# Kernel tuning notes

Hardware: AMD Instinct MI355X
Metric: run time of the kernel (lower is better)

The kernel has to match this reference:

```python
import jax, jax.numpy as jnp
import numpy as np

N_NODES = 100000
N_EDGES = 1600000
IN_F = 128
HID_F = 128
OUT_F = 128
HEAD_HID = 128
HEAD_OUT = 64


def setup_inputs() -> dict:
    key = jax.random.key(0)
    ks = jax.random.split(key, 16)
    glorot = lambda k, i, o: jax.random.normal(k, (i, o), jnp.float32) * (2.0 / (i + o)) ** 0.5
    return {
        "x": jax.random.normal(ks[0], (N_NODES, IN_F), jnp.float32),
        "src": jax.random.randint(ks[1], (N_EDGES,), 0, N_NODES),
        "dst": jax.random.randint(ks[2], (N_EDGES,), 0, N_NODES),
        "eps1": jnp.zeros((), jnp.float32),
        "eps2": jnp.zeros((), jnp.float32),
        # mlp_fun1: in_feats -> hid -> hid
        "w11": glorot(ks[3], IN_F, HID_F), "b11": jnp.zeros((HID_F,), jnp.float32),
        "w12": glorot(ks[4], HID_F, HID_F), "b12": jnp.zeros((HID_F,), jnp.float32),
        # mlp_fun2: hid -> hid -> out_feats
        "w21": glorot(ks[5], HID_F, HID_F), "b21": jnp.zeros((HID_F,), jnp.float32),
        "w22": glorot(ks[6], HID_F, OUT_F), "b22": jnp.zeros((OUT_F,), jnp.float32),
        # head mlp: out_feats -> hidden_dim -> output_dim (sigmoid)
        "wm1": glorot(ks[7], OUT_F, HEAD_HID), "bm1": jnp.zeros((HEAD_HID,), jnp.float32),
        "wm2": glorot(ks[8], HEAD_HID, HEAD_OUT), "bm2": jnp.zeros((HEAD_OUT,), jnp.float32),
    }


def _mlp2(h, w1, b1, w2, b2):
    # 2-layer MLP: Linear -> ReLU -> Linear
    return jax.nn.relu(h @ w1 + b1) @ w2 + b2


def _gin_conv(x, src, dst, eps, w1, b1, w2, b2):
    # sum-aggregate over incoming edges, then MLP update (DGL GINConv, learn_eps)
    agg = jax.ops.segment_sum(x[src], dst, num_segments=x.shape[0])  # [N, d]
    return _mlp2((1.0 + eps) * x + agg, w1, b1, w2, b2)


def reference(x, src, dst, eps1, eps2, w11, b11, w12, b12,
              w21, b21, w22, b22, wm1, bm1, wm2, bm2):
    # dropout is identity in eval mode
    h = jax.nn.relu(_gin_conv(x, src, dst, eps1, w11, b11, w12, b12))
    h = jax.nn.relu(_gin_conv(h, src, dst, eps2, w21, b21, w22, b22))
    # head MLP producing per-node probabilities (consumed by log-prob loss)
    return jax.nn.sigmoid(_mlp2(h, wm1, bm1, wm2, bm2))  # [N, output_dim]
```

## Files before the change

kernel.cpp:

```cpp
#include <hip/hip_runtime.h>

static constexpr int NN = 100000;
static constexpr int NE = 1600000;
static constexpr int NBUK = (NN + 255) / 256;
static constexpr int SC_BLOCKS = 400;
static constexpr int SC_CH = NE / SC_BLOCKS;

typedef float     f32x4  __attribute__((ext_vector_type(4)));
typedef _Float16  f16x8  __attribute__((ext_vector_type(8)));

static constexpr float LO_SCALE  = 16384.0f;
static constexpr float LO_USCALE = 1.0f / 16384.0f;

__device__ __forceinline__ unsigned pkh(float x, float y){
  unsigned short a = __builtin_bit_cast(unsigned short, (_Float16)x);
  unsigned short b = __builtin_bit_cast(unsigned short, (_Float16)y);
  return (unsigned)a | ((unsigned)b << 16);
}
__device__ __forceinline__ float2 uph(unsigned u){
  _Float16 a = __builtin_bit_cast(_Float16, (unsigned short)(u & 0xffffu));
  _Float16 b = __builtin_bit_cast(_Float16, (unsigned short)(u >> 16));
  return make_float2((float)a, (float)b);
}

__global__ void k_pack(const float* __restrict__ w11, const float* __restrict__ w12,
                       const float* __restrict__ w21, const float* __restrict__ w22,
                       const float* __restrict__ wm1, const float* __restrict__ wm2,
                       unsigned short* __restrict__ p11, unsigned short* __restrict__ p12,
                       unsigned short* __restrict__ p21, unsigned short* __restrict__ p22,
                       unsigned short* __restrict__ pm1, unsigned short* __restrict__ pm2){
  int b = blockIdx.x, lane = threadIdx.x;
  const float* W; unsigned short* P; int NCT, f;
  if (b < 160){
    int m = b >> 5; f = b & 31; NCT = 8;
    W = (m==0)?w11:(m==1)?w12:(m==2)?w21:(m==3)?w22:wm1;
    P = (m==0)?p11:(m==1)?p12:(m==2)?p21:(m==3)?p22:pm1;
  } else { f = b - 160; NCT = 4; W = wm2; P = pm2; }
  int NC = NCT * 16;
  int kt = f / NCT, ct = f % NCT;
  int hidx = ct >> 2, ct4 = ct & 3;
  int k0 = kt*32 + ((lane>>4)*8), col = ct*16 + (lane&15);
  unsigned short* dh = P + (hidx<<14) + ((kt*4+ct4)<<10) + (lane<<3);
  unsigned short* dl = dh + 512;
  #pragma unroll
  for (int j=0;j<8;j++){
    float v = W[(size_t)(k0+j)*NC + col];
    _Float16 h = (_Float16)v;
    _Float16 l = (_Float16)((v - (float)h) * LO_SCALE);
    dh[j] = __builtin_bit_cast(unsigned short, h);
    dl[j] = __builtin_bit_cast(unsigned short, l);
  }
}

__global__ void k_cvt(const float* __restrict__ x, unsigned* __restrict__ xh, int n4){
  int i = blockIdx.x*256 + threadIdx.x;
  if (i < n4){
    float4 v = reinterpret_cast<const float4*>(x)[i];
    uint2 o; o.x = pkh(v.x, v.y); o.y = pkh(v.z, v.w);
    reinterpret_cast<uint2*>(xh)[i] = o;
  }
}

__global__ __launch_bounds__(256) void k_hist(const int* __restrict__ dst, int* __restrict__ bhist){
  __shared__ int h[NBUK];
  int blk = blockIdx.x, t = threadIdx.x;
  for (int i=t;i<NBUK;i+=256) h[i]=0;
  __syncthreads();
  int e0 = blk*SC_CH;
  for (int e=e0+t; e<e0+SC_CH; e+=256) atomicAdd(&h[((unsigned)dst[e])>>8], 1);
  __syncthreads();
  for (int i=t;i<NBUK;i+=256){ int c=h[i]; if (c) atomicAdd(&bhist[i], c); }
}

__global__ void k_boff2(const int* __restrict__ bhist, int* __restrict__ boff){
  __shared__ int s[512];
  int t = threadIdx.x;
  int v = (t < NBUK) ? bhist[t] : 0;
  s[t] = v; __syncthreads();
  for (int off=1; off<512; off<<=1){
    int u = 0; if (t>=off) u = s[t-off];
    __syncthreads(); s[t] += u; __syncthreads();
  }
  if (t < NBUK) boff[t] = s[t] - v;
}

__global__ __launch_bounds__(256) void k_scatter1(const int* __restrict__ src,
                                                  const int* __restrict__ dst,
                                                  const int* __restrict__ boff,
                                                  int* __restrict__ gbcur,
                                                  uint2* __restrict__ tmp){
  __shared__ int hc[NBUK];
  __shared__ int hb[NBUK];
  int blk = blockIdx.x, t = threadIdx.x;
  int e0 = blk * SC_CH, e1 = e0 + SC_CH;
  for (int i=t;i<NBUK;i+=256) hc[i]=0;
  __syncthreads();
  for (int e=e0+t; e<e1; e+=256) atomicAdd(&hc[((unsigned)dst[e])>>8], 1);
  __syncthreads();
  for (int i=t;i<NBUK;i+=256){ int c = hc[i]; hb[i] = c ? atomicAdd(&gbcur[i], c) : 0; }
  __syncthreads();
  for (int i=t;i<NBUK;i+=256) hc[i]=0;
  __syncthreads();
  for (int e=e0+t; e<e1; e+=256){
    int d = dst[e]; int b = ((unsigned)d)>>8;
    int pos = atomicAdd(&hc[b], 1);
    tmp[(size_t)boff[b] + hb[b] + pos] = make_uint2((unsigned)src[e], (unsigned)d);
  }
}

__global__ __launch_bounds__(256) void k_fill2(const uint2* __restrict__ tmp,
                                               const int* __restrict__ boff,
                                               const int* __restrict__ bhist,
                                               int* __restrict__ eidx,
                                               int* __restrict__ rs, int* __restrict__ deg, int N){
  __shared__ int lh[256];
  __shared__ int ls[256];
  __shared__ int lc[256];
  int b = blockIdx.x, t = threadIdx.x;
  int base = boff[b], cnt = bhist[b];
  int nb0 = b*256;
  lh[t] = 0; lc[t] = 0;
  __syncthreads();
  for (int i=t; i<cnt; i+=256) atomicAdd(&lh[(int)tmp[(size_t)base+i].y - nb0], 1);
  __syncthreads();
  int v = lh[t];
  ls[t] = v; __syncthreads();
  for (int off=1; off<256; off<<=1){
    int u = 0; if (t>=off) u = ls[t-off];
    __syncthreads(); ls[t] += u; __syncthreads();
  }
  int node = nb0 + t;
  if (node < N){ deg[node] = v; rs[node] = base + ls[t] - v; }
  __syncthreads();
  for (int i=t; i<cnt; i+=256){
    uint2 e = tmp[(size_t)base+i];
    int local = (int)e.y - nb0;
    int pos = atomicAdd(&lc[local], 1);
    eidx[base + ls[local] - lh[local] + pos] = (int)e.x;
  }
}

__global__ __launch_bounds__(256) void k_agg(const unsigned* __restrict__ inp,
                                             unsigned* __restrict__ out,
                                             const float* __restrict__ epsp,
                                             const int* __restrict__ rs, const int* __restrict__ deg,
                                             const int* __restrict__ eidx, int N){
  int gw = (blockIdx.x*256 + threadIdx.x) >> 6;
  int lane = threadIdx.x & 63;
  if (gw >= N) return;
  float sc = 1.0f + *epsp;
  float2 v = uph(inp[(size_t)gw*64 + lane]);
  float a0 = sc * v.x, a1 = sc * v.y;
  int beg = rs[gw], d = deg[gw];
  int i = 0;
  for (; i+8 <= d; i += 8){
    unsigned u[8];
    #pragma unroll
    for (int j=0;j<8;j++) u[j] = inp[(size_t)eidx[beg+i+j]*64 + lane];
    #pragma unroll
    for (int j=0;j<8;j++){ float2 f = uph(u[j]); a0 += f.x; a1 += f.y; }
  }
  for (; i < d; ++i){
    float2 u = uph(inp[(size_t)eidx[beg+i]*64 + lane]);
    a0 += u.x; a1 += u.y;
  }
  out[(size_t)gw*64 + lane] = pkh(a0, a1);
}

static constexpr int HSTR = 136;
static constexpr int WSLICE = 32*HSTR;

__device__ __forceinline__ void load_a_glob2(const _Float16* __restrict__ t, int rbase,
                                             int lane, int N, f16x8 a[2][4]){
  #pragma unroll
  for (int ms=0; ms<2; ++ms){
    int row = rbase + ms*16 + (lane & 15); if (row >= N) row = N - 1;
    const _Float16* ap = t + (size_t)row*128 + ((lane>>4)*8);
    #pragma unroll
    for (int kt=0;kt<4;kt++) a[ms][kt] = *reinterpret_cast<const f16x8*>(ap + kt*32);
  }
}
__device__ __forceinline__ void load_a_lds2(const _Float16* slice, int lane, f16x8 a[2][4]){
  int ko = (lane>>4)*8;
  #pragma unroll
  for (int ms=0; ms<2; ++ms){
    const _Float16* rp = slice + (ms*16 + (lane&15))*HSTR + ko;
    #pragma unroll
    for (int kt=0;kt<4;kt++) a[ms][kt] = *reinterpret_cast<const f16x8*>(rp + kt*32);
  }
}

__device__ __forceinline__ void half_relu(const f16x8 a[2][4],
                                          const unsigned short* __restrict__ w,
                                          const float* __restrict__ bias,
                                          _Float16* slice, int lane, int hidx){
  const unsigned short* wb = w + (hidx<<14);
  int r0 = (lane>>4)*4, col0 = lane & 15;
  #pragma unroll
  for (int ct4=0; ct4<4; ++ct4){
    f32x4 c0={0.f,0.f,0.f,0.f}, c1={0.f,0.f,0.f,0.f};
    f32x4 d0={0.f,0.f,0.f,0.f}, d1={0.f,0.f,0.f,0.f};
    #pragma unroll
    for (int kt=0; kt<4; ++kt){
      const f16x8 bh = *reinterpret_cast<const f16x8*>(wb + ((kt*4+ct4)<<10) + (lane<<3));
      const f16x8 bl = *reinterpret_cast<const f16x8*>(wb + ((kt*4+ct4)<<10) + 512 + (lane<<3));
      c0 = __builtin_amdgcn_mfma_f32_16x16x32_f16(a[0][kt], bh, c0, 0,0,0);
      c1 = __builtin_amdgcn_mfma_f32_16x16x32_f16(a[1][kt], bh, c1, 0,0,0);
      d0 = __builtin_amdgcn_mfma_f32_16x16x32_f16(a[0][kt], bl, d0, 0,0,0);
      d1 = __builtin_amdgcn_mfma_f32_16x16x32_f16(a[1][kt], bl, d1, 0,0,0);
    }
    float bv = bias[hidx*64 + ct4*16 + col0];
    int cb = hidx*64 + ct4*16 + col0;
    #pragma unroll
    for (int r=0;r<4;r++){
      float v0 = fmaxf(c0[r] + d0[r]*LO_USCALE + bv, 0.f);
      float v1 = fmaxf(c1[r] + d1[r]*LO_USCALE + bv, 0.f);
      slice[(r0+r)*HSTR + cb]      = (_Float16)v0;
      slice[(16+r0+r)*HSTR + cb]   = (_Float16)v1;
    }
  }
}

__device__ __forceinline__ void head_sig(const f16x8 a[2][4],
                                         const unsigned short* __restrict__ w,
                                         const float* __restrict__ bias,
                                         float* fs, int lane){
  int r0 = (lane>>4)*4, col0 = lane & 15;
  #pragma unroll
  for (int ct4=0; ct4<4; ++ct4){
    f32x4 c0={0.f,0.f,0.f,0.f}, c1={0.f,0.f,0.f,0.f};
    f32x4 d0={0.f,0.f,0.f,0.f}, d1={0.f,0.f,0.f,0.f};
    #pragma unroll
    for (int kt=0; kt<4; ++kt){
      const f16x8 bh = *reinterpret_cast<const f16x8*>(w + ((kt*4+ct4)<<10) + (lane<<3));
      const f16x8 bl = *reinterpret_cast<const f16x8*>(w + ((kt*4+ct4)<<10) + 512 + (lane<<3));
      c0 = __builtin_amdgcn_mfma_f32_16x16x32_f16(a[0][kt], bh, c0, 0,0,0);
      c1 = __builtin_amdgcn_mfma_f32_16x16x32_f16(a[1][kt], bh, c1, 0,0,0);
      d0 = __builtin_amdgcn_mfma_f32_16x16x32_f16(a[0][kt], bl, d0, 0,0,0);
      d1 = __builtin_amdgcn_mfma_f32_16x16x32_f16(a[1][kt], bl, d1, 0,0,0);
    }
    float bv = bias[ct4*16 + col0];
    int cb = ct4*16 + col0;
    #pragma unroll
    for (int r=0;r<4;r++){
      float z0 = c0[r] + d0[r]*LO_USCALE + bv;
      float z1 = c1[r] + d1[r]*LO_USCALE + bv;
      fs[(r0+r)*68 + cb]    = 1.0f / (1.0f + __expf(-z0));
      fs[(16+r0+r)*68 + cb] = 1.0f / (1.0f + __expf(-z1));
    }
  }
}

__global__ __launch_bounds__(256) void k_mlp1(const _Float16* __restrict__ t,
    const unsigned short* __restrict__ w1, const float* __restrict__ b1,
    const unsigned short* __restrict__ w2, const float* __restrict__ b2,
    unsigned* __restrict__ h, int N){
  __shared__ _Float16 lds[4*WSLICE];
  int tid = threadIdx.x, lane = tid & 63, wv = tid >> 6;
  _Float16* slice = lds + wv*WSLICE;
  int rbase = blockIdx.x*128 + wv*32;
  f16x8 a[2][4];
  load_a_glob2(t, rbase, lane, N, a);
  half_relu(a, w1, b1, slice, lane, 0);
  half_relu(a, w1, b1, slice, lane, 1);
  load_a_lds2(slice, lane, a);
  half_relu(a, w2, b2, slice, lane, 0);
  half_relu(a, w2, b2, slice, lane, 1);
  for (int i=lane; i < 32*32; i += 64){
    int r = i >> 5, c = i & 31;
    if (rbase + r < N)
      reinterpret_cast<uint2*>(h)[(size_t)(rbase + r)*32 + c] =
        *reinterpret_cast<const uint2*>(slice + r*HSTR + c*4);
  }
}

__global__ __launch_bounds__(256) void k_mlp2_head(const _Float16* __restrict__ t,
    const unsigned short* __restrict__ w1, const float* __restrict__ b1,
    const unsigned short* __restrict__ w2, const float* __restrict__ b2,
    const unsigned short* __restrict__ w3, const float* __restrict__ b3,
    const unsigned short* __restrict__ w4, const float* __restrict__ b4,
    float* __restrict__ out, int N){
  __shared__ _Float16 lds[4*WSLICE];
  int tid = threadIdx.x, lane = tid & 63, wv = tid >> 6;
  _Float16* slice = lds + wv*WSLICE;
  int rbase = blockIdx.x*128 + wv*32;
  f16x8 a[2][4];
  load_a_glob2(t, rbase, lane, N, a);
  half_relu(a, w1, b1, slice, lane, 0);
  half_relu(a, w1, b1, slice, lane, 1);
  load_a_lds2(slice, lane, a);
  half_relu(a, w2, b2, slice, lane, 0);
  half_relu(a, w2, b2, slice, lane, 1);
  load_a_lds2(slice, lane, a);
  half_relu(a, w3, b3, slice, lane, 0);
  half_relu(a, w3, b3, slice, lane, 1);
  load_a_lds2(slice, lane, a);
  float* fs = reinterpret_cast<float*>(slice);
  head_sig(a, w4, b4, fs, lane);
  for (int i=lane; i < 32*16; i += 64){
    int r = i >> 4, c = i & 15;
    if (rbase + r < N)
      reinterpret_cast<float4*>(out)[(size_t)(rbase + r)*16 + c] =
        *reinterpret_cast<const float4*>(fs + r*68 + c*4);
  }
}

extern "C" void kernel_launch(void* const* d_in, const int* in_sizes, int n_in,
                              void* d_out, int out_size, void* d_ws, size_t ws_size,
                              hipStream_t stream) {
  const float* x   = (const float*)d_in[0];
  const int*   src = (const int*)  d_in[1];
  const int*   dst = (const int*)  d_in[2];
  const float* eps1= (const float*)d_in[3];
  const float* eps2= (const float*)d_in[4];
  const float* w11 = (const float*)d_in[5];  const float* b11 = (const float*)d_in[6];
  const float* w12 = (const float*)d_in[7];  const float* b12 = (const float*)d_in[8];
  const float* w21 = (const float*)d_in[9];  const float* b21 = (const float*)d_in[10];
  const float* w22 = (const float*)d_in[11]; const float* b22 = (const float*)d_in[12];
  const float* wm1 = (const float*)d_in[13]; const float* bm1 = (const float*)d_in[14];
  const float* wm2 = (const float*)d_in[15]; const float* bm2 = (const float*)d_in[16];

  char* ws = (char*)d_ws;
  size_t off = 0;
  auto alloc = [&](size_t bytes) -> void* {
    void* p = ws + off;
    off = (off + bytes + 255) & ~(size_t)255;
    return p;
  };
  unsigned* xh  = (unsigned*)alloc((size_t)NN*64*4);
  unsigned* B0  = (unsigned*)alloc((size_t)NN*64*4);
  unsigned* h1h = (unsigned*)alloc((size_t)NN*64*4);
  uint2* tmp = (uint2*)alloc((size_t)NE*8);
  int* eidx = (int*)alloc((size_t)NE*4);
  int* deg  = (int*)alloc((size_t)NN*4);
  int* rs   = (int*)alloc((size_t)NN*4);
  int* bhist= (int*)alloc((size_t)NBUK*4);
  int* boff = (int*)alloc((size_t)NBUK*4);
  int* gbcur= (int*)alloc((size_t)NBUK*4);
  unsigned short* p11 = (unsigned short*)alloc(128*128*2*2);
  unsigned short* p12 = (unsigned short*)alloc(128*128*2*2);
  unsigned short* p21 = (unsigned short*)alloc(128*128*2*2);
  unsigned short* p22 = (unsigned short*)alloc(128*128*2*2);
  unsigned short* pm1 = (unsigned short*)alloc(128*128*2*2);
  unsigned short* pm2 = (unsigned short*)alloc(128*64*2*2);
  if (off > ws_size) return;

  hipMemsetAsync(bhist, 0, (size_t)NBUK*4, stream);
  hipMemsetAsync(gbcur, 0, (size_t)NBUK*4, stream);

  k_pack<<<176, 64, 0, stream>>>(w11,w12,w21,w22,wm1,wm2, p11,p12,p21,p22,pm1,pm2);
  k_cvt<<<(NN*32 + 255)/256, 256, 0, stream>>>(x, xh, NN*32);
  k_hist<<<SC_BLOCKS, 256, 0, stream>>>(dst, bhist);
  k_boff2<<<1, 512, 0, stream>>>(bhist, boff);
  k_scatter1<<<SC_BLOCKS, 256, 0, stream>>>(src, dst, boff, gbcur, tmp);
  k_fill2<<<NBUK, 256, 0, stream>>>(tmp, boff, bhist, eidx, rs, deg, NN);

  int mgrid = (NN + 127) / 128;
  k_agg<<<(NN+3)/4, 256, 0, stream>>>(xh, B0, eps1, rs, deg, eidx, NN);
  k_mlp1<<<mgrid, 256, 0, stream>>>((const _Float16*)B0, p11, b11, p12, b12, h1h, NN);
  k_agg<<<(NN+3)/4, 256, 0, stream>>>(h1h, B0, eps2, rs, deg, eidx, NN);
  k_mlp2_head<<<mgrid, 256, 0, stream>>>((const _Float16*)B0, p21, b21, p22, b22,
                                         pm1, bm1, pm2, bm2, (float*)d_out, NN);
}
```

Before: 301.2 us.

## Fuse neighbor aggregation into MLP kernels and pack scatter entries to 32 bits

Each wave now gathers and sums neighbor rows for its 32 nodes directly into its LDS slice, then runs the MLP on that slice. This removes the separate aggregation kernels and the fp16 intermediate buffer round trip through global memory. The scatter temp array also packs src<<8 with the low 8 bits of dst into one 32-bit word, halving that traffic. The trade-off is fewer waves doing the latency-bound gather: one wave per 32 nodes instead of one per node, serialized over m, which may expose memory latency.

```diff
diff --git a/kernel.cpp b/kernel.cpp
--- a/kernel.cpp
+++ b/kernel.cpp
@@ -88,7 +88,7 @@
                                                   const int* __restrict__ dst,
                                                   const int* __restrict__ boff,
                                                   int* __restrict__ gbcur,
-                                                  uint2* __restrict__ tmp){
+                                                  unsigned* __restrict__ tmp){
   __shared__ int hc[NBUK];
   __shared__ int hb[NBUK];
   int blk = blockIdx.x, t = threadIdx.x;
@@ -102,13 +102,13 @@
   for (int i=t;i<NBUK;i+=256) hc[i]=0;
   __syncthreads();
   for (int e=e0+t; e<e1; e+=256){
-    int d = dst[e]; int b = ((unsigned)d)>>8;
+    unsigned d = (unsigned)dst[e]; unsigned b = d>>8;
     int pos = atomicAdd(&hc[b], 1);
-    tmp[(size_t)boff[b] + hb[b] + pos] = make_uint2((unsigned)src[e], (unsigned)d);
-  }
-}
-
-__global__ __launch_bounds__(256) void k_fill2(const uint2* __restrict__ tmp,
+    tmp[(size_t)boff[b] + hb[b] + pos] = ((unsigned)src[e] << 8) | (d & 255u);
+  }
+}
+
+__global__ __launch_bounds__(256) void k_fill2(const unsigned* __restrict__ tmp,
                                                const int* __restrict__ boff,
                                                const int* __restrict__ bhist,
                                                int* __restrict__ eidx,
@@ -118,10 +118,9 @@
   __shared__ int lc[256];
   int b = blockIdx.x, t = threadIdx.x;
   int base = boff[b], cnt = bhist[b];
-  int nb0 = b*256;
   lh[t] = 0; lc[t] = 0;
   __syncthreads();
-  for (int i=t; i<cnt; i+=256) atomicAdd(&lh[(int)tmp[(size_t)base+i].y - nb0], 1);
+  for (int i=t; i<cnt; i+=256) atomicAdd(&lh[tmp[(size_t)base+i] & 255u], 1);
   __syncthreads();
   int v = lh[t];
   ls[t] = v; __syncthreads();
@@ -129,29 +128,25 @@
     int u = 0; if (t>=off) u = ls[t-off];
     __syncthreads(); ls[t] += u; __syncthreads();
   }
-  int node = nb0 + t;
+  int node = b*256 + t;
   if (node < N){ deg[node] = v; rs[node] = base + ls[t] - v; }
   __syncthreads();
   for (int i=t; i<cnt; i+=256){
-    uint2 e = tmp[(size_t)base+i];
-    int local = (int)e.y - nb0;
+    unsigned e = tmp[(size_t)base+i];
+    int local = e & 255u;
     int pos = atomicAdd(&lc[local], 1);
-    eidx[base + ls[local] - lh[local] + pos] = (int)e.x;
-  }
-}
-
-__global__ __launch_bounds__(256) void k_agg(const unsigned* __restrict__ inp,
-                                             unsigned* __restrict__ out,
-                                             const float* __restrict__ epsp,
-                                             const int* __restrict__ rs, const int* __restrict__ deg,
-                                             const int* __restrict__ eidx, int N){
-  int gw = (blockIdx.x*256 + threadIdx.x) >> 6;
-  int lane = threadIdx.x & 63;
-  if (gw >= N) return;
-  float sc = 1.0f + *epsp;
-  float2 v = uph(inp[(size_t)gw*64 + lane]);
+    eidx[base + ls[local] - lh[local] + pos] = (int)(e >> 8);
+  }
+}
+
+static constexpr int HSTR = 136;
+static constexpr int WSLICE = 32*HSTR;
+
+__device__ __forceinline__ float2 gather_row(const unsigned* __restrict__ inp, float sc,
+                                             int beg, int d, const int* __restrict__ eidx,
+                                             int node, int lane){
+  float2 v = uph(inp[(size_t)node*64 + lane]);
   float a0 = sc * v.x, a1 = sc * v.y;
-  int beg = rs[gw], d = deg[gw];
   int i = 0;
   for (; i+8 <= d; i += 8){
     unsigned u[8];
@@ -164,22 +159,24 @@
     float2 u = uph(inp[(size_t)eidx[beg+i]*64 + lane]);
     a0 += u.x; a1 += u.y;
   }
-  out[(size_t)gw*64 + lane] = pkh(a0, a1);
-}
-
-static constexpr int HSTR = 136;
-static constexpr int WSLICE = 32*HSTR;
-
-__device__ __forceinline__ void load_a_glob2(const _Float16* __restrict__ t, int rbase,
-                                             int lane, int N, f16x8 a[2][4]){
-  #pragma unroll
-  for (int ms=0; ms<2; ++ms){
-    int row = rbase + ms*16 + (lane & 15); if (row >= N) row = N - 1;
-    const _Float16* ap = t + (size_t)row*128 + ((lane>>4)*8);
-    #pragma unroll
-    for (int kt=0;kt<4;kt++) a[ms][kt] = *reinterpret_cast<const f16x8*>(ap + kt*32);
-  }
-}
+  return make_float2(a0, a1);
+}
+
+__device__ __forceinline__ void gather32(const unsigned* __restrict__ inp, float sc,
+                                         const int* __restrict__ rs, const int* __restrict__ deg,
+                                         const int* __restrict__ eidx,
+                                         int nbase, int lane, int N, _Float16* slice){
+  for (int m=0; m<32; ++m){
+    int node = nbase + m;
+    unsigned o = 0;
+    if (node < N){
+      float2 r = gather_row(inp, sc, rs[node], deg[node], eidx, node, lane);
+      o = pkh(r.x, r.y);
+    }
+    *reinterpret_cast<unsigned*>(slice + m*HSTR + lane*2) = o;
+  }
+}
+
 __device__ __forceinline__ void load_a_lds2(const _Float16* slice, int lane, f16x8 a[2][4]){
   int ko = (lane>>4)*8;
   #pragma unroll
@@ -251,7 +248,9 @@
   }
 }
 
-__global__ __launch_bounds__(256) void k_mlp1(const _Float16* __restrict__ t,
+__global__ __launch_bounds__(256) void k_fused1(const unsigned* __restrict__ inp,
+    const float* __restrict__ epsp,
+    const int* __restrict__ rs, const int* __restrict__ deg, const int* __restrict__ eidx,
     const unsigned short* __restrict__ w1, const float* __restrict__ b1,
     const unsigned short* __restrict__ w2, const float* __restrict__ b2,
     unsigned* __restrict__ h, int N){
@@ -259,8 +258,10 @@
   int tid = threadIdx.x, lane = tid & 63, wv = tid >> 6;
   _Float16* slice = lds + wv*WSLICE;
   int rbase = blockIdx.x*128 + wv*32;
+  float sc = 1.0f + *epsp;
+  gather32(inp, sc, rs, deg, eidx, rbase, lane, N, slice);
   f16x8 a[2][4];
-  load_a_glob2(t, rbase, lane, N, a);
+  load_a_lds2(slice, lane, a);
   half_relu(a, w1, b1, slice, lane, 0);
   half_relu(a, w1, b1, slice, lane, 1);
   load_a_lds2(slice, lane, a);
@@ -274,7 +275,9 @@
   }
 }
 
-__global__ __launch_bounds__(256) void k_mlp2_head(const _Float16* __restrict__ t,
+__global__ __launch_bounds__(256) void k_fused2(const unsigned* __restrict__ inp,
+    const float* __restrict__ epsp,
+    const int* __restrict__ rs, const int* __restrict__ deg, const int* __restrict__ eidx,
     const unsigned short* __restrict__ w1, const float* __restrict__ b1,
     const unsigned short* __restrict__ w2, const float* __restrict__ b2,
     const unsigned short* __restrict__ w3, const float* __restrict__ b3,
@@ -284,8 +287,10 @@
   int tid = threadIdx.x, lane = tid & 63, wv = tid >> 6;
   _Float16* slice = lds + wv*WSLICE;
   int rbase = blockIdx.x*128 + wv*32;
+  float sc = 1.0f + *epsp;
+  gather32(inp, sc, rs, deg, eidx, rbase, lane, N, slice);
   f16x8 a[2][4];
-  load_a_glob2(t, rbase, lane, N, a);
+  load_a_lds2(slice, lane, a);
   half_relu(a, w1, b1, slice, lane, 0);
   half_relu(a, w1, b1, slice, lane, 1);
   load_a_lds2(slice, lane, a);
@@ -328,9 +333,8 @@
     return p;
   };
   unsigned* xh  = (unsigned*)alloc((size_t)NN*64*4);
-  unsigned* B0  = (unsigned*)alloc((size_t)NN*64*4);
   unsigned* h1h = (unsigned*)alloc((size_t)NN*64*4);
-  uint2* tmp = (uint2*)alloc((size_t)NE*8);
+  unsigned* tmp = (unsigned*)alloc((size_t)NE*4);
   int* eidx = (int*)alloc((size_t)NE*4);
   int* deg  = (int*)alloc((size_t)NN*4);
   int* rs   = (int*)alloc((size_t)NN*4);
@@ -356,9 +360,9 @@
   k_fill2<<<NBUK, 256, 0, stream>>>(tmp, boff, bhist, eidx, rs, deg, NN);
 
   int mgrid = (NN + 127) / 128;
-  k_agg<<<(NN+3)/4, 256, 0, stream>>>(xh, B0, eps1, rs, deg, eidx, NN);
-  k_mlp1<<<mgrid, 256, 0, stream>>>((const _Float16*)B0, p11, b11, p12, b12, h1h, NN);
-  k_agg<<<(NN+3)/4, 256, 0, stream>>>(h1h, B0, eps2, rs, deg, eidx, NN);
-  k_mlp2_head<<<mgrid, 256, 0, stream>>>((const _Float16*)B0, p21, b21, p22, b22,
-                                         pm1, bm1, pm2, bm2, (float*)d_out, NN);
-}
+  k_fused1<<<mgrid, 256, 0, stream>>>(xh, eps1, rs, deg, eidx,
+                                      p11, b11, p12, b12, h1h, NN);
+  k_fused2<<<mgrid, 256, 0, stream>>>(h1h, eps2, rs, deg, eidx,
+                                      p21, b21, p22, b22, pm1, bm1, pm2, bm2,
+                                      (float*)d_out, NN);
+}
```

Measured after the change: 381.5 us. 26.7% more time.

## Split aggregation into column groups and pack edge tmp into one word

Applied to the files above, without the earlier changes.

The aggregation kernel is restructured so each block handles one of eight 32-byte column slices for 32 nodes, with 8 lanes per node. Blocks working on the same column slice then touch a smaller working set of the feature table, which is meant to improve L2 cache reuse during the random gathers. The CSR build also packs the source index and the low 8 bits of the destination into one 32-bit word, halving the temp buffer traffic. The trade-offs are narrower 32-byte gather segments per row, redundant edge-index reads across the eight column groups, and a packing that assumes source indices fit in 24 bits.

```diff
diff --git a/kernel.cpp b/kernel.cpp
--- a/kernel.cpp
+++ b/kernel.cpp
@@ -88,7 +88,7 @@
                                                   const int* __restrict__ dst,
                                                   const int* __restrict__ boff,
                                                   int* __restrict__ gbcur,
-                                                  uint2* __restrict__ tmp){
+                                                  unsigned* __restrict__ tmp){
   __shared__ int hc[NBUK];
   __shared__ int hb[NBUK];
   int blk = blockIdx.x, t = threadIdx.x;
@@ -102,13 +102,13 @@
   for (int i=t;i<NBUK;i+=256) hc[i]=0;
   __syncthreads();
   for (int e=e0+t; e<e1; e+=256){
-    int d = dst[e]; int b = ((unsigned)d)>>8;
+    unsigned d = (unsigned)dst[e]; unsigned b = d>>8;
     int pos = atomicAdd(&hc[b], 1);
-    tmp[(size_t)boff[b] + hb[b] + pos] = make_uint2((unsigned)src[e], (unsigned)d);
-  }
-}
-
-__global__ __launch_bounds__(256) void k_fill2(const uint2* __restrict__ tmp,
+    tmp[(size_t)boff[b] + hb[b] + pos] = ((unsigned)src[e] << 8) | (d & 255u);
+  }
+}
+
+__global__ __launch_bounds__(256) void k_fill2(const unsigned* __restrict__ tmp,
                                                const int* __restrict__ boff,
                                                const int* __restrict__ bhist,
                                                int* __restrict__ eidx,
@@ -118,10 +118,9 @@
   __shared__ int lc[256];
   int b = blockIdx.x, t = threadIdx.x;
   int base = boff[b], cnt = bhist[b];
-  int nb0 = b*256;
   lh[t] = 0; lc[t] = 0;
   __syncthreads();
-  for (int i=t; i<cnt; i+=256) atomicAdd(&lh[(int)tmp[(size_t)base+i].y - nb0], 1);
+  for (int i=t; i<cnt; i+=256) atomicAdd(&lh[tmp[(size_t)base+i] & 255u], 1);
   __syncthreads();
   int v = lh[t];
   ls[t] = v; __syncthreads();
@@ -129,42 +128,46 @@
     int u = 0; if (t>=off) u = ls[t-off];
     __syncthreads(); ls[t] += u; __syncthreads();
   }
-  int node = nb0 + t;
+  int node = b*256 + t;
   if (node < N){ deg[node] = v; rs[node] = base + ls[t] - v; }
   __syncthreads();
   for (int i=t; i<cnt; i+=256){
-    uint2 e = tmp[(size_t)base+i];
-    int local = (int)e.y - nb0;
+    unsigned e = tmp[(size_t)base+i];
+    int local = e & 255u;
     int pos = atomicAdd(&lc[local], 1);
-    eidx[base + ls[local] - lh[local] + pos] = (int)e.x;
-  }
-}
-
-__global__ __launch_bounds__(256) void k_agg(const unsigned* __restrict__ inp,
-                                             unsigned* __restrict__ out,
-                                             const float* __restrict__ epsp,
-                                             const int* __restrict__ rs, const int* __restrict__ deg,
-                                             const int* __restrict__ eidx, int N){
-  int gw = (blockIdx.x*256 + threadIdx.x) >> 6;
-  int lane = threadIdx.x & 63;
-  if (gw >= N) return;
+    eidx[base + ls[local] - lh[local] + pos] = (int)(e >> 8);
+  }
+}
+
+__global__ __launch_bounds__(256) void k_agg_col(const unsigned* __restrict__ inp,
+                                                 unsigned* __restrict__ out,
+                                                 const float* __restrict__ epsp,
+                                                 const int* __restrict__ rs, const int* __restrict__ deg,
+                                                 const int* __restrict__ eidx, int N){
+  int colg = blockIdx.x & 7;
+  int nb   = blockIdx.x >> 3;
+  int tid = threadIdx.x, wv = tid >> 6, lane = tid & 63;
+  int sub = lane >> 3, w = lane & 7;
+  int node = nb*32 + wv*8 + sub;
+  if (node >= N) return;
   float sc = 1.0f + *epsp;
-  float2 v = uph(inp[(size_t)gw*64 + lane]);
+  const unsigned* base = inp + colg*8 + w;
+  float2 v = uph(base[(size_t)node*64]);
   float a0 = sc * v.x, a1 = sc * v.y;
-  int beg = rs[gw], d = deg[gw];
+  int beg = rs[node], d = deg[node];
   int i = 0;
   for (; i+8 <= d; i += 8){
     unsigned u[8];
     #pragma unroll
-    for (int j=0;j<8;j++) u[j] = inp[(size_t)eidx[beg+i+j]*64 + lane];
+    for (int j=0;j<8;j++) u[j] = base[(size_t)eidx[beg+i+j]*64];
     #pragma unroll
     for (int j=0;j<8;j++){ float2 f = uph(u[j]); a0 += f.x; a1 += f.y; }
   }
   for (; i < d; ++i){
-    float2 u = uph(inp[(size_t)eidx[beg+i]*64 + lane]);
+    float2 u = uph(base[(size_t)eidx[beg+i]*64]);
     a0 += u.x; a1 += u.y;
   }
-  out[(size_t)gw*64 + lane] = pkh(a0, a1);
+  out[(size_t)node*64 + colg*8 + w] = pkh(a0, a1);
 }
 
 static constexpr int HSTR = 136;
@@ -330,7 +333,7 @@
   unsigned* xh  = (unsigned*)alloc((size_t)NN*64*4);
   unsigned* B0  = (unsigned*)alloc((size_t)NN*64*4);
   unsigned* h1h = (unsigned*)alloc((size_t)NN*64*4);
-  uint2* tmp = (uint2*)alloc((size_t)NE*8);
+  unsigned* tmp = (unsigned*)alloc((size_t)NE*4);
   int* eidx = (int*)alloc((size_t)NE*4);
   int* deg  = (int*)alloc((size_t)NN*4);
   int* rs   = (int*)alloc((size_t)NN*4);
@@ -355,10 +358,11 @@
   k_scatter1<<<SC_BLOCKS, 256, 0, stream>>>(src, dst, boff, gbcur, tmp);
   k_fill2<<<NBUK, 256, 0, stream>>>(tmp, boff, bhist, eidx, rs, deg, NN);
 
+  int agrid = 8 * ((NN + 31) / 32);
   int mgrid = (NN + 127) / 128;
-  k_agg<<<(NN+3)/4, 256, 0, stream>>>(xh, B0, eps1, rs, deg, eidx, NN);
+  k_agg_col<<<agrid, 256, 0, stream>>>(xh, B0, eps1, rs, deg, eidx, NN);
   k_mlp1<<<mgrid, 256, 0, stream>>>((const _Float16*)B0, p11, b11, p12, b12, h1h, NN);
-  k_agg<<<(NN+3)/4, 256, 0, stream>>>(h1h, B0, eps2, rs, deg, eidx, NN);
+  k_agg_col<<<agrid, 256, 0, stream>>>(h1h, B0, eps2, rs, deg, eidx, NN);
   k_mlp2_head<<<mgrid, 256, 0, stream>>>((const _Float16*)B0, p21, b21, p22, b22,
                                          pm1, bm1, pm2, bm2, (float*)d_out, NN);
 }
```

Result: slower. 541.6 us (+79.8%).
